# Optimization experiments

Measured on AMD Instinct MI355X. Metric: run time of the kernel, lower is better.

Reference implementation:

```python
import jax, jax.numpy as jnp
import numpy as np

B, T, C, H = 4, 2048, 1024, 16
HD = C // H  # head dim = 64


def setup_inputs() -> dict:
    key = jax.random.key(0)
    ks = jax.random.split(key, 5)
    s = 1.0 / np.sqrt(C)
    return {
        "x": jax.random.normal(ks[0], (B, T, C), jnp.float32),
        "Wk": jax.random.normal(ks[1], (C, C), jnp.float32) * s,
        "bk": jnp.zeros((C,), jnp.float32),
        "Wq": jax.random.normal(ks[2], (C, C), jnp.float32) * s,
        "bq": jnp.zeros((C,), jnp.float32),
        "Wv": jax.random.normal(ks[3], (C, C), jnp.float32) * s,
        "bv": jnp.zeros((C,), jnp.float32),
        "Wp": jax.random.normal(ks[4], (C, C), jnp.float32) * s,
        "bp": jnp.zeros((C,), jnp.float32),
    }


def reference(x, Wk, bk, Wq, bq, Wv, bv, Wp, bp):
    # Linear(in, out): y = x @ W.T + b  (W stored as [out, in], torch convention)
    k = (x @ Wk.T + bk).reshape(B, T, H, HD).transpose(0, 2, 1, 3)  # [B,H,T,HD]
    q = (x @ Wq.T + bq).reshape(B, T, H, HD).transpose(0, 2, 1, 3)
    v = (x @ Wv.T + bv).reshape(B, T, H, HD).transpose(0, 2, 1, 3)
    scale = 1.0 / np.sqrt(HD)
    att = jnp.einsum("bhqd,bhkd->bhqk", q, k) * scale  # [B,H,T,T]
    causal = jnp.tril(jnp.ones((T, T), bool))
    att = jnp.where(causal[None, None, :, :], att, -jnp.inf)
    att = jax.nn.softmax(att, axis=-1)
    y = jnp.einsum("bhqk,bhkd->bhqd", att, v)  # [B,H,T,HD]
    y = y.transpose(0, 2, 1, 3).reshape(B, T, C)
    return y @ Wp.T + bp
```

## Files before the change

### kernel.cpp

```cpp
#include <hip/hip_runtime.h>
#include <hip/hip_bf16.h>
#include <cmath>

#define Tt 2048
#define Cc 1024
#define Hh 16
#define HDd 64

typedef __attribute__((ext_vector_type(8))) short short8;
typedef __attribute__((ext_vector_type(4))) float f32x4;

#define ASYNC16(gp, lp)                                       \
    __builtin_amdgcn_global_load_lds(                         \
        (const __attribute__((address_space(1))) void*)(gp),  \
        (__attribute__((address_space(3))) void*)(lp), 16, 0, 0)

__device__ __forceinline__ unsigned short f32_bf16(float f) {
    unsigned u = __float_as_uint(f);
    u += 0x7FFF + ((u >> 16) & 1);
    return (unsigned short)(u >> 16);
}
__device__ __forceinline__ unsigned short f32_bf16_rn(float f) {
    return (unsigned short)((__float_as_uint(f) + 0x8000u) >> 16);
}
__device__ __forceinline__ float fast_exp2(float x) {
#if __has_builtin(__builtin_amdgcn_exp2f)
    return __builtin_amdgcn_exp2f(x);
#else
    return exp2f(x);
#endif
}

__global__ __launch_bounds__(256) void cvt_all(
    const float* __restrict__ x, const float* __restrict__ a,
    const float* __restrict__ b, const float* __restrict__ c,
    const float* __restrict__ d, unsigned short* __restrict__ ox,
    unsigned short* __restrict__ oa, unsigned short* __restrict__ ob,
    unsigned short* __restrict__ oc, unsigned short* __restrict__ od) {
    const int id = blockIdx.x * 256 + threadIdx.x;
    const float* src; unsigned short* dst; int sub;
    if (id < 2097152) {
        src = x; dst = ox; sub = id;
    } else {
        const int wi = id - 2097152;
        const int which = wi >> 18;
        sub = wi & 262143;
        if (which == 0)      { src = a; dst = oa; }
        else if (which == 1) { src = b; dst = ob; }
        else if (which == 2) { src = c; dst = oc; }
        else                 { src = d; dst = od; }
    }
    float4 v = ((const float4*)src)[sub];
    ushort4 o;
    o.x = f32_bf16(v.x); o.y = f32_bf16(v.y);
    o.z = f32_bf16(v.z); o.w = f32_bf16(v.w);
    ((ushort4*)dst)[sub] = o;
}

__global__ __launch_bounds__(256) void gemm_qkv(const unsigned short* __restrict__ A,
                                                const unsigned short* __restrict__ Wcat,
                                                const float* __restrict__ bq,
                                                const float* __restrict__ bk,
                                                const float* __restrict__ bv,
                                                unsigned short* __restrict__ qout,
                                                unsigned short* __restrict__ kout,
                                                unsigned short* __restrict__ vout) {
    __shared__ unsigned short sA[2][128 * 32];
    __shared__ unsigned short sB[2][128 * 32];

    const int tid  = threadIdx.x;
    const int bm0  = blockIdx.y * 128;
    const int bn0  = blockIdx.x * 128;
    const int wid  = tid >> 6;
    const int lane = tid & 63;
    const int quad = lane >> 4;
    const int lr   = lane & 15;
    const int wm   = (wid & 1) * 64;
    const int wn   = (wid >> 1) * 64;

    const int sr   = lane >> 2;
    const int scol = (lane & 3) * 8;
    const int row0 = wid * 16 + sr;
    const int row1 = 64 + wid * 16 + sr;
    const int lo0  = wid * 512;
    const int lo1  = (4 + wid) * 512;

    f32x4 acc[4][4];
    f32x4 zero = {0.f, 0.f, 0.f, 0.f};
#pragma unroll
    for (int i = 0; i < 4; i++)
#pragma unroll
        for (int j = 0; j < 4; j++) acc[i][j] = zero;

    ASYNC16(A    + (size_t)(bm0 + row0) * Cc + scol, sA[0] + lo0);
    ASYNC16(A    + (size_t)(bm0 + row1) * Cc + scol, sA[0] + lo1);
    ASYNC16(Wcat + (size_t)(bn0 + row0) * Cc + scol, sB[0] + lo0);
    ASYNC16(Wcat + (size_t)(bn0 + row1) * Cc + scol, sB[0] + lo1);
    __syncthreads();

    for (int kt = 0; kt < Cc / 32; ++kt) {
        const int cur = kt & 1, nxt = cur ^ 1;
        if (kt + 1 < Cc / 32) {
            const int kb = (kt + 1) * 32;
            ASYNC16(A    + (size_t)(bm0 + row0) * Cc + kb + scol, sA[nxt] + lo0);
            ASYNC16(A    + (size_t)(bm0 + row1) * Cc + kb + scol, sA[nxt] + lo1);
            ASYNC16(Wcat + (size_t)(bn0 + row0) * Cc + kb + scol, sB[nxt] + lo0);
            ASYNC16(Wcat + (size_t)(bn0 + row1) * Cc + kb + scol, sB[nxt] + lo1);
        }

        short8 af[4], bf[4];
#pragma unroll
        for (int i = 0; i < 4; i++)
            af[i] = *(const short8*)(sA[cur] + (wm + i * 16 + lr) * 32 + quad * 8);
#pragma unroll
        for (int j = 0; j < 4; j++)
            bf[j] = *(const short8*)(sB[cur] + (wn + j * 16 + lr) * 32 + quad * 8);
#pragma unroll
        for (int i = 0; i < 4; i++)
#pragma unroll
            for (int j = 0; j < 4; j++)
                acc[i][j] = __builtin_amdgcn_mfma_f32_16x16x32_bf16(af[i], bf[j], acc[i][j], 0, 0, 0);

        __syncthreads();
    }

    const int which = bn0 >> 10;
    const float* bias = (which == 0) ? bq : (which == 1) ? bk : bv;
    unsigned short* outp = (which == 0) ? qout : (which == 1) ? kout : vout;
    const float scale = (which == 0) ? 0.1803368801111204f : 1.0f;
    const bool vmode = (which == 2);
    const int nb = bn0 & 1023;

#pragma unroll
    for (int j = 0; j < 4; j++) {
        const int nl = nb + wn + j * 16 + lr;
        const float bvv = bias[nl];
        const int h = nl >> 6, hd = nl & 63;
#pragma unroll
        for (int i = 0; i < 4; i++) {
            const int m0 = bm0 + wm + i * 16 + quad * 4;
            const int b = m0 >> 11, t0 = m0 & 2047;
            if (vmode) {
                ushort4 pk;
                pk.x = f32_bf16_rn(acc[i][j][0] + bvv);
                pk.y = f32_bf16_rn(acc[i][j][1] + bvv);
                pk.z = f32_bf16_rn(acc[i][j][2] + bvv);
                pk.w = f32_bf16_rn(acc[i][j][3] + bvv);
                *(ushort4*)(outp + (((size_t)(b * Hh + h)) * HDd + hd) * Tt + t0) = pk;
            } else {
#pragma unroll
                for (int r = 0; r < 4; r++) {
                    const float val = (acc[i][j][r] + bvv) * scale;
                    outp[(((size_t)(b * Hh + h)) * Tt + t0 + r) * HDd + hd] =
                        f32_bf16_rn(val);
                }
            }
        }
    }
}

__global__ __launch_bounds__(256) void gemm_proj(const unsigned short* __restrict__ A,
                                                 const unsigned short* __restrict__ W,
                                                 const float* __restrict__ bias,
                                                 float* __restrict__ out) {
    __shared__ unsigned short sA[2][128 * 32];
    __shared__ unsigned short sB[2][64 * 32];

    const int tid  = threadIdx.x;
    const int bm0  = blockIdx.y * 128;
    const int bn0  = blockIdx.x * 64;
    const int wid  = tid >> 6;
    const int lane = tid & 63;
    const int quad = lane >> 4;
    const int lr   = lane & 15;
    const int wm   = (wid & 1) * 64;
    const int wn   = (wid >> 1) * 32;

    const int sr   = lane >> 2;
    const int scol = (lane & 3) * 8;
    const int row0 = wid * 16 + sr;
    const int row1 = 64 + wid * 16 + sr;
    const int lo0  = wid * 512;
    const int lo1  = (4 + wid) * 512;

    f32x4 acc[4][2];
    f32x4 zero = {0.f, 0.f, 0.f, 0.f};
#pragma unroll
    for (int i = 0; i < 4; i++)
#pragma unroll
        for (int j = 0; j < 2; j++) acc[i][j] = zero;

    ASYNC16(A + (size_t)(bm0 + row0) * Cc + scol, sA[0] + lo0);
    ASYNC16(A + (size_t)(bm0 + row1) * Cc + scol, sA[0] + lo1);
    ASYNC16(W + (size_t)(bn0 + row0) * Cc + scol, sB[0] + lo0);
    __syncthreads();

    for (int kt = 0; kt < Cc / 32; ++kt) {
        const int cur = kt & 1, nxt = cur ^ 1;
        if (kt + 1 < Cc / 32) {
            const int kb = (kt + 1) * 32;
            ASYNC16(A + (size_t)(bm0 + row0) * Cc + kb + scol, sA[nxt] + lo0);
            ASYNC16(A + (size_t)(bm0 + row1) * Cc + kb + scol, sA[nxt] + lo1);
            ASYNC16(W + (size_t)(bn0 + row0) * Cc + kb + scol, sB[nxt] + lo0);
        }

        short8 af[4], bf[2];
#pragma unroll
        for (int i = 0; i < 4; i++)
            af[i] = *(const short8*)(sA[cur] + (wm + i * 16 + lr) * 32 + quad * 8);
#pragma unroll
        for (int j = 0; j < 2; j++)
            bf[j] = *(const short8*)(sB[cur] + (wn + j * 16 + lr) * 32 + quad * 8);
#pragma unroll
        for (int i = 0; i < 4; i++)
#pragma unroll
            for (int j = 0; j < 2; j++)
                acc[i][j] = __builtin_amdgcn_mfma_f32_16x16x32_bf16(af[i], bf[j], acc[i][j], 0, 0, 0);

        __syncthreads();
    }

#pragma unroll
    for (int j = 0; j < 2; j++) {
        const int n = bn0 + wn + j * 16 + lr;
        const float bvv = bias[n];
#pragma unroll
        for (int i = 0; i < 4; i++)
#pragma unroll
            for (int r = 0; r < 4; r++) {
                const int m = bm0 + wm + i * 16 + quad * 4 + r;
                out[(size_t)m * Cc + n] = acc[i][j][r] + bvv;
            }
    }
}

__global__ __launch_bounds__(256) void attn(const unsigned short* __restrict__ q,
                                            const unsigned short* __restrict__ k,
                                            const unsigned short* __restrict__ vt,
                                            unsigned short* __restrict__ y) {
    __shared__ unsigned short sK[2][64 * 72];
    __shared__ unsigned short sV[2][64 * 72];
    __shared__ unsigned short sP[4][2][16 * 72];

    const int tid  = threadIdx.x;
    const int wid  = tid >> 6;
    const int lane = tid & 63;
    const int quad = lane >> 4;
    const int lr   = lane & 15;

    const int bh = blockIdx.y;
    const size_t headq = (size_t)bh * Tt * HDd;
    const unsigned short* kg = k + headq;
    const unsigned short* vg = vt + headq;
    const int b = bh >> 4, h = bh & 15;

    const int rs0 = tid >> 3;
    const int es  = (tid & 7) * 8;

    f32x4 zero = {0.f, 0.f, 0.f, 0.f};

    for (int pass = 0; pass < 2; ++pass) {
        const int qt = pass ? (15 - blockIdx.x) : blockIdx.x;
        const int qb = qt * 128;
        const int ntiles = 2 * qt + 2;

        short8 qf[2][2];
#pragma unroll
        for (int s = 0; s < 2; s++) {
            const unsigned short* qp =
                q + headq + (size_t)(qb + s * 64 + wid * 16 + lr) * HDd;
            qf[s][0] = *(const short8*)(qp + quad * 8);
            qf[s][1] = *(const short8*)(qp + 32 + quad * 8);
        }

        f32x4 o[2][4];
        float l_run[2][4];
#pragma unroll
        for (int s = 0; s < 2; s++)
#pragma unroll
            for (int i = 0; i < 4; i++) { o[s][i] = zero; l_run[s][i] = 0.f; }

        uint4 ka0 = *(const uint4*)(kg + (size_t)(rs0)      * HDd + es);
        uint4 ka1 = *(const uint4*)(kg + (size_t)(rs0 + 32) * HDd + es);
        uint4 va0 = *(const uint4*)(vg + (size_t)(rs0)      * Tt + es);
        uint4 va1 = *(const uint4*)(vg + (size_t)(rs0 + 32) * Tt + es);
        *(uint4*)(sK[0] + rs0 * 72 + es)        = ka0;
        *(uint4*)(sK[0] + (rs0 + 32) * 72 + es) = ka1;
        *(uint4*)(sV[0] + rs0 * 72 + es)        = va0;
        *(uint4*)(sV[0] + (rs0 + 32) * 72 + es) = va1;
        __syncthreads();
        {
            const int kb2 = 64;
            ka0 = *(const uint4*)(kg + (size_t)(kb2 + rs0)      * HDd + es);
            ka1 = *(const uint4*)(kg + (size_t)(kb2 + rs0 + 32) * HDd + es);
            va0 = *(const uint4*)(vg + (size_t)(rs0)      * Tt + kb2 + es);
            va1 = *(const uint4*)(vg + (size_t)(rs0 + 32) * Tt + kb2 + es);
        }

        for (int kt = 0; kt < ntiles; ++kt) {
            const int cur = kt & 1, nxt = cur ^ 1;
            if (kt + 1 < ntiles) {
                *(uint4*)(sK[nxt] + rs0 * 72 + es)        = ka0;
                *(uint4*)(sK[nxt] + (rs0 + 32) * 72 + es) = ka1;
                *(uint4*)(sV[nxt] + rs0 * 72 + es)        = va0;
                *(uint4*)(sV[nxt] + (rs0 + 32) * 72 + es) = va1;
            }
            if (kt + 2 < ntiles) {
                const int kb2 = (kt + 2) * 64;
                ka0 = *(const uint4*)(kg + (size_t)(kb2 + rs0)      * HDd + es);
                ka1 = *(const uint4*)(kg + (size_t)(kb2 + rs0 + 32) * HDd + es);
                va0 = *(const uint4*)(vg + (size_t)(rs0)      * Tt + kb2 + es);
                va1 = *(const uint4*)(vg + (size_t)(rs0 + 32) * Tt + kb2 + es);
            }

            const unsigned short* bK = sK[cur];
            const unsigned short* bV = sV[cur];
            const int s_lo = (kt == ntiles - 1) ? 1 : 0;

            f32x4 sc[2][4];
#pragma unroll
            for (int s = 0; s < 2; s++) {
                if (s < s_lo) continue;
#pragma unroll
                for (int nt = 0; nt < 4; nt++) {
                    short8 b0 = *(const short8*)(bK + (nt * 16 + lr) * 72 + quad * 8);
                    short8 b1 = *(const short8*)(bK + (nt * 16 + lr) * 72 + 32 + quad * 8);
                    f32x4 a = zero;
                    a = __builtin_amdgcn_mfma_f32_16x16x32_bf16(qf[s][0], b0, a, 0, 0, 0);
                    a = __builtin_amdgcn_mfma_f32_16x16x32_bf16(qf[s][1], b1, a, 0, 0, 0);
                    sc[s][nt] = a;
                }
            }

#pragma unroll
            for (int s = 0; s < 2; s++) {
                if (s < s_lo) continue;
                if (kt == ntiles - 2 + s) {
#pragma unroll
                    for (int nt = 0; nt < 4; nt++)
#pragma unroll
                        for (int r = 0; r < 4; r++)
                            sc[s][nt][r] = (nt * 16 + lr <= wid * 16 + quad * 4 + r)
                                               ? sc[s][nt][r] : -INFINITY;
                }
                unsigned short* sPw = sP[wid][s];
#pragma unroll
                for (int nt = 0; nt < 4; nt++)
#pragma unroll
                    for (int r = 0; r < 4; r++) {
                        const float p = fast_exp2(sc[s][nt][r]);
                        l_run[s][r] += p;
                        sPw[(quad * 4 + r) * 72 + nt * 16 + lr] = f32_bf16_rn(p);
                    }
            }

#pragma unroll
            for (int s = 0; s < 2; s++) {
                if (s < s_lo) continue;
                const unsigned short* sPw = sP[wid][s];
                short8 pa0 = *(const short8*)(sPw + lr * 72 + quad * 8);
                short8 pa1 = *(const short8*)(sPw + lr * 72 + 32 + quad * 8);
#pragma unroll
                for (int nt = 0; nt < 4; nt++) {
                    short8 vb0 = *(const short8*)(bV + (nt * 16 + lr) * 72 + quad * 8);
                    short8 vb1 = *(const short8*)(bV + (nt * 16 + lr) * 72 + 32 + quad * 8);
                    o[s][nt] = __builtin_amdgcn_mfma_f32_16x16x32_bf16(pa0, vb0, o[s][nt], 0, 0, 0);
                    o[s][nt] = __builtin_amdgcn_mfma_f32_16x16x32_bf16(pa1, vb1, o[s][nt], 0, 0, 0);
                }
            }

            __syncthreads();
        }

#pragma unroll
        for (int s = 0; s < 2; s++) {
#pragma unroll
            for (int r = 0; r < 4; r++) {
                float ls = l_run[s][r];
                ls += __shfl_xor(ls, 1);
                ls += __shfl_xor(ls, 2);
                ls += __shfl_xor(ls, 4);
                ls += __shfl_xor(ls, 8);
                const float inv = 1.0f / ls;
                const int t = qb + s * 64 + wid * 16 + quad * 4 + r;
#pragma unroll
                for (int nt = 0; nt < 4; nt++) {
                    const int dim = nt * 16 + lr;
                    y[((size_t)(b * Tt + t)) * Cc + h * HDd + dim] =
                        f32_bf16_rn(o[s][nt][r] * inv);
                }
            }
        }
    }
}

extern "C" void kernel_launch(void* const* d_in, const int* in_sizes, int n_in,
                              void* d_out, int out_size, void* d_ws, size_t ws_size,
                              hipStream_t stream) {
    const float* x  = (const float*)d_in[0];
    const float* Wk = (const float*)d_in[1];
    const float* bk = (const float*)d_in[2];
    const float* Wq = (const float*)d_in[3];
    const float* bq = (const float*)d_in[4];
    const float* Wv = (const float*)d_in[5];
    const float* bv = (const float*)d_in[6];
    const float* Wp = (const float*)d_in[7];
    const float* bp = (const float*)d_in[8];
    float* out = (float*)d_out;

    char* ws = (char*)d_ws;
    size_t off = 0;
    auto alloc = [&](size_t bytes) { char* p = ws + off; off += bytes; return p; };
    const size_t MK = (size_t)8192 * 1024;
    const size_t NK = (size_t)1024 * 1024;
    unsigned short* xb   = (unsigned short*)alloc(MK * 2);
    unsigned short* Wcat = (unsigned short*)alloc(3 * NK * 2);
    unsigned short* Wqb  = Wcat;
    unsigned short* Wkb  = Wcat + NK;
    unsigned short* Wvb  = Wcat + 2 * NK;
    unsigned short* Wpb  = (unsigned short*)alloc(NK * 2);
    unsigned short* qh   = (unsigned short*)alloc(MK * 2);
    unsigned short* kh   = (unsigned short*)alloc(MK * 2);
    unsigned short* vth  = (unsigned short*)alloc(MK * 2);
    unsigned short* ya   = (unsigned short*)alloc(MK * 2);

    cvt_all<<<12288, 256, 0, stream>>>(x, Wq, Wk, Wv, Wp, xb, Wqb, Wkb, Wvb, Wpb);

    gemm_qkv<<<dim3(24, 64), 256, 0, stream>>>(xb, Wcat, bq, bk, bv, qh, kh, vth);

    attn<<<dim3(8, 64), 256, 0, stream>>>(qh, kh, vth, ya);

    gemm_proj<<<dim3(16, 64), 256, 0, stream>>>(ya, Wpb, bp, out);
}
```

Measured before the change: 279.3 us.

## Rewrite QKV GEMM as 256x256 eight-wave pipelined kernel with swizzled LDS

Replaces the 128x128 four-wave QKV projection GEMM with a 256x256 tile, 512-thread kernel that uses K-steps of 64 and 128KB of dynamic LDS double-buffered in four quadrants. Global-to-LDS loads are interleaved with four MFMA phases under explicit barriers, s_setprio and waitcnt control. LDS columns are XOR-swizzled to avoid bank conflicts. The aim is more data reuse per byte loaded and better overlap of memory with MFMA work. The cost is higher register pressure and only 384 blocks, which could leave some CUs idle.

```diff
diff --git a/kernel.cpp b/kernel.cpp
--- a/kernel.cpp
+++ b/kernel.cpp
@@ -57,72 +57,142 @@
     ((ushort4*)dst)[sub] = o;
 }
 
-__global__ __launch_bounds__(256) void gemm_qkv(const unsigned short* __restrict__ A,
-                                                const unsigned short* __restrict__ Wcat,
-                                                const float* __restrict__ bq,
-                                                const float* __restrict__ bk,
-                                                const float* __restrict__ bv,
-                                                unsigned short* __restrict__ qout,
-                                                unsigned short* __restrict__ kout,
-                                                unsigned short* __restrict__ vout) {
-    __shared__ unsigned short sA[2][128 * 32];
-    __shared__ unsigned short sB[2][128 * 32];
+__global__ __launch_bounds__(512, 2) void gemm_qkv8(
+    const unsigned short* __restrict__ A,
+    const unsigned short* __restrict__ Wcat,
+    const float* __restrict__ bq, const float* __restrict__ bk,
+    const float* __restrict__ bv,
+    unsigned short* __restrict__ qout, unsigned short* __restrict__ kout,
+    unsigned short* __restrict__ vout) {
+    extern __shared__ unsigned short lds[];
 
     const int tid  = threadIdx.x;
-    const int bm0  = blockIdx.y * 128;
-    const int bn0  = blockIdx.x * 128;
     const int wid  = tid >> 6;
     const int lane = tid & 63;
     const int quad = lane >> 4;
     const int lr   = lane & 15;
-    const int wm   = (wid & 1) * 64;
-    const int wn   = (wid >> 1) * 64;
-
-    const int sr   = lane >> 2;
-    const int scol = (lane & 3) * 8;
-    const int row0 = wid * 16 + sr;
-    const int row1 = 64 + wid * 16 + sr;
-    const int lo0  = wid * 512;
-    const int lo1  = (4 + wid) * 512;
-
-    f32x4 acc[4][4];
-    f32x4 zero = {0.f, 0.f, 0.f, 0.f};
-#pragma unroll
-    for (int i = 0; i < 4; i++)
-#pragma unroll
-        for (int j = 0; j < 4; j++) acc[i][j] = zero;
-
-    ASYNC16(A    + (size_t)(bm0 + row0) * Cc + scol, sA[0] + lo0);
-    ASYNC16(A    + (size_t)(bm0 + row1) * Cc + scol, sA[0] + lo1);
-    ASYNC16(Wcat + (size_t)(bn0 + row0) * Cc + scol, sB[0] + lo0);
-    ASYNC16(Wcat + (size_t)(bn0 + row1) * Cc + scol, sB[0] + lo1);
-    __syncthreads();
-
-    for (int kt = 0; kt < Cc / 32; ++kt) {
-        const int cur = kt & 1, nxt = cur ^ 1;
-        if (kt + 1 < Cc / 32) {
-            const int kb = (kt + 1) * 32;
-            ASYNC16(A    + (size_t)(bm0 + row0) * Cc + kb + scol, sA[nxt] + lo0);
-            ASYNC16(A    + (size_t)(bm0 + row1) * Cc + kb + scol, sA[nxt] + lo1);
-            ASYNC16(Wcat + (size_t)(bn0 + row0) * Cc + kb + scol, sB[nxt] + lo0);
-            ASYNC16(Wcat + (size_t)(bn0 + row1) * Cc + kb + scol, sB[nxt] + lo1);
-        }
-
-        short8 af[4], bf[4];
-#pragma unroll
-        for (int i = 0; i < 4; i++)
-            af[i] = *(const short8*)(sA[cur] + (wm + i * 16 + lr) * 32 + quad * 8);
-#pragma unroll
-        for (int j = 0; j < 4; j++)
-            bf[j] = *(const short8*)(sB[cur] + (wn + j * 16 + lr) * 32 + quad * 8);
-#pragma unroll
-        for (int i = 0; i < 4; i++)
-#pragma unroll
-            for (int j = 0; j < 4; j++)
-                acc[i][j] = __builtin_amdgcn_mfma_f32_16x16x32_bf16(af[i], bf[j], acc[i][j], 0, 0, 0);
-
-        __syncthreads();
-    }
+    const int wr   = wid >> 2;
+    const int wc   = wid & 3;
+
+    const int bm0 = blockIdx.y * 256;
+    const int bn0 = blockIdx.x * 256;
+
+    const int srow  = wid * 8 + (lane >> 3);
+    const int scol  = ((lane & 7) ^ (lane >> 3)) * 8;
+    const int sldso = wid * 512;
+
+    const int a_r   = wr * 64 + lr;
+    const int b_r   = wc * 32 + lr;
+    const int slot0 = (quad ^ (lr & 7)) * 8;
+    const int slot1 = ((quad ^ 4) ^ (lr & 7)) * 8;
+
+    f32x4 acc[8][4];
+    const f32x4 zero = {0.f, 0.f, 0.f, 0.f};
+#pragma unroll
+    for (int i = 0; i < 8; ++i)
+#pragma unroll
+        for (int j = 0; j < 4; ++j) acc[i][j] = zero;
+
+    short8 areg[4][2];
+    short8 breg[2][2][2];
+
+#define STG(S, BUF, REG, GB, GROW)                                          \
+    do {                                                                    \
+        if ((S) < 16) {                                                     \
+            unsigned short* lb = lds + ((BUF) * 4 + (REG)) * 8192 + sldso;  \
+            const unsigned short* gp =                                      \
+                (GB) + (size_t)((GROW) + srow) * Cc + (S) * 64 + scol;      \
+            ASYNC16(gp, lb);                                                \
+            ASYNC16(gp + (size_t)64 * Cc, lb + 4096);                       \
+        }                                                                   \
+    } while (0)
+
+#define LDA(mh)                                                             \
+    do {                                                                    \
+        const unsigned short* ab = bufb + (mh) * 8192;                      \
+        _Pragma("unroll") for (int mf = 0; mf < 4; ++mf) {                  \
+            areg[mf][0] = *(const short8*)(ab + (a_r + mf * 16) * 64 + slot0); \
+            areg[mf][1] = *(const short8*)(ab + (a_r + mf * 16) * 64 + slot1); \
+        }                                                                   \
+    } while (0)
+
+#define LDB(nh)                                                             \
+    do {                                                                    \
+        const unsigned short* bb = bufb + (2 + (nh)) * 8192;                \
+        _Pragma("unroll") for (int nf = 0; nf < 2; ++nf) {                  \
+            breg[nh][nf][0] = *(const short8*)(bb + (b_r + nf * 16) * 64 + slot0); \
+            breg[nh][nf][1] = *(const short8*)(bb + (b_r + nf * 16) * 64 + slot1); \
+        }                                                                   \
+    } while (0)
+
+#define MFMA_PHASE(mh, nh)                                                  \
+    _Pragma("unroll") for (int mf = 0; mf < 4; ++mf)                        \
+    _Pragma("unroll") for (int nf = 0; nf < 2; ++nf) {                      \
+        acc[(mh)*4+mf][(nh)*2+nf] = __builtin_amdgcn_mfma_f32_16x16x32_bf16( \
+            areg[mf][0], breg[nh][nf][0], acc[(mh)*4+mf][(nh)*2+nf], 0,0,0); \
+        acc[(mh)*4+mf][(nh)*2+nf] = __builtin_amdgcn_mfma_f32_16x16x32_bf16( \
+            areg[mf][1], breg[nh][nf][1], acc[(mh)*4+mf][(nh)*2+nf], 0,0,0); \
+    }
+
+#define TILE(T, BC, WN)                                                     \
+    {                                                                       \
+        const unsigned short* bufb = lds + (BC) * 32768;                    \
+        LDA(0);                                                             \
+        LDB(0);                                                             \
+        STG((T) + 1, (BC) ^ 1, 1, A, bm0 + 128);                            \
+        __builtin_amdgcn_s_barrier();                                       \
+        asm volatile("s_waitcnt lgkmcnt(0)" ::: "memory");                  \
+        __builtin_amdgcn_s_setprio(1);                                      \
+        MFMA_PHASE(0, 0);                                                   \
+        __builtin_amdgcn_s_setprio(0);                                      \
+        __builtin_amdgcn_s_barrier();                                       \
+        LDB(1);                                                             \
+        STG((T) + 1, (BC) ^ 1, 3, Wcat, bn0 + 128);                         \
+        __builtin_amdgcn_s_barrier();                                       \
+        asm volatile("s_waitcnt lgkmcnt(0)" ::: "memory");                  \
+        __builtin_amdgcn_s_setprio(1);                                      \
+        MFMA_PHASE(0, 1);                                                   \
+        __builtin_amdgcn_s_setprio(0);                                      \
+        __builtin_amdgcn_s_barrier();                                       \
+        LDA(1);                                                             \
+        STG((T) + 2, (BC), 0, A, bm0);                                      \
+        __builtin_amdgcn_s_barrier();                                       \
+        asm volatile("s_waitcnt lgkmcnt(0)" ::: "memory");                  \
+        __builtin_amdgcn_s_setprio(1);                                      \
+        MFMA_PHASE(1, 0);                                                   \
+        __builtin_amdgcn_s_setprio(0);                                      \
+        __builtin_amdgcn_s_barrier();                                       \
+        STG((T) + 2, (BC), 2, Wcat, bn0);                                   \
+        __builtin_amdgcn_s_barrier();                                       \
+        __builtin_amdgcn_s_setprio(1);                                      \
+        MFMA_PHASE(1, 1);                                                   \
+        __builtin_amdgcn_s_setprio(0);                                      \
+        asm volatile("s_waitcnt vmcnt(" #WN ")" ::: "memory");              \
+        __builtin_amdgcn_s_barrier();                                       \
+    }
+
+    STG(0, 0, 0, A, bm0);
+    STG(0, 0, 1, A, bm0 + 128);
+    STG(0, 0, 2, Wcat, bn0);
+    STG(0, 0, 3, Wcat, bn0 + 128);
+    STG(1, 1, 0, A, bm0);
+    STG(1, 1, 2, Wcat, bn0);
+    asm volatile("s_waitcnt vmcnt(4)" ::: "memory");
+    __builtin_amdgcn_s_barrier();
+
+    for (int t2 = 0; t2 < 7; ++t2) {
+        const int T0 = t2 * 2;
+        TILE(T0, 0, 4);
+        TILE(T0 + 1, 1, 4);
+    }
+    TILE(14, 0, 0);
+    TILE(15, 1, 0);
+
+#undef TILE
+#undef MFMA_PHASE
+#undef LDB
+#undef LDA
+#undef STG
 
     const int which = bn0 >> 10;
     const float* bias = (which == 0) ? bq : (which == 1) ? bk : bv;
@@ -132,31 +202,35 @@
     const int nb = bn0 & 1023;
 
 #pragma unroll
-    for (int j = 0; j < 4; j++) {
-        const int nl = nb + wn + j * 16 + lr;
-        const float bvv = bias[nl];
-        const int h = nl >> 6, hd = nl & 63;
-#pragma unroll
-        for (int i = 0; i < 4; i++) {
-            const int m0 = bm0 + wm + i * 16 + quad * 4;
-            const int b = m0 >> 11, t0 = m0 & 2047;
-            if (vmode) {
-                ushort4 pk;
-                pk.x = f32_bf16_rn(acc[i][j][0] + bvv);
-                pk.y = f32_bf16_rn(acc[i][j][1] + bvv);
-                pk.z = f32_bf16_rn(acc[i][j][2] + bvv);
-                pk.w = f32_bf16_rn(acc[i][j][3] + bvv);
-                *(ushort4*)(outp + (((size_t)(b * Hh + h)) * HDd + hd) * Tt + t0) = pk;
-            } else {
-#pragma unroll
-                for (int r = 0; r < 4; r++) {
-                    const float val = (acc[i][j][r] + bvv) * scale;
-                    outp[(((size_t)(b * Hh + h)) * Tt + t0 + r) * HDd + hd] =
-                        f32_bf16_rn(val);
+    for (int nh = 0; nh < 2; ++nh)
+#pragma unroll
+        for (int nf = 0; nf < 2; ++nf) {
+            const int nl = nb + nh * 128 + wc * 32 + nf * 16 + lr;
+            const float bvv = bias[nl];
+            const int h = nl >> 6, hd = nl & 63;
+#pragma unroll
+            for (int mh = 0; mh < 2; ++mh)
+#pragma unroll
+                for (int mf = 0; mf < 4; ++mf) {
+                    const f32x4 a = acc[mh * 4 + mf][nh * 2 + nf];
+                    const int m0 = bm0 + mh * 128 + wr * 64 + mf * 16 + quad * 4;
+                    const int b = m0 >> 11, t0 = m0 & 2047;
+                    if (vmode) {
+                        ushort4 pk;
+                        pk.x = f32_bf16_rn(a[0] + bvv);
+                        pk.y = f32_bf16_rn(a[1] + bvv);
+                        pk.z = f32_bf16_rn(a[2] + bvv);
+                        pk.w = f32_bf16_rn(a[3] + bvv);
+                        *(ushort4*)(outp + (((size_t)(b * Hh + h)) * HDd + hd) * Tt + t0) = pk;
+                    } else {
+#pragma unroll
+                        for (int r = 0; r < 4; ++r) {
+                            outp[(((size_t)(b * Hh + h)) * Tt + t0 + r) * HDd + hd] =
+                                f32_bf16_rn((a[r] + bvv) * scale);
+                        }
+                    }
                 }
-            }
         }
-    }
 }
 
 __global__ __launch_bounds__(256) void gemm_proj(const unsigned short* __restrict__ A,
@@ -424,9 +498,17 @@
     unsigned short* vth  = (unsigned short*)alloc(MK * 2);
     unsigned short* ya   = (unsigned short*)alloc(MK * 2);
 
+    static bool lds_attr_set = false;
+    if (!lds_attr_set) {
+        (void)hipFuncSetAttribute((const void*)gemm_qkv8,
+                                  hipFuncAttributeMaxDynamicSharedMemorySize,
+                                  131072);
+        lds_attr_set = true;
+    }
+
     cvt_all<<<12288, 256, 0, stream>>>(x, Wq, Wk, Wv, Wp, xb, Wqb, Wkb, Wvb, Wpb);
 
-    gemm_qkv<<<dim3(24, 64), 256, 0, stream>>>(xb, Wcat, bq, bk, bv, qh, kh, vth);
+    gemm_qkv8<<<dim3(12, 32), 512, 131072, stream>>>(xb, Wcat, bq, bk, bv, qh, kh, vth);
 
     attn<<<dim3(8, 64), 256, 0, stream>>>(qh, kh, vth, ya);
 
```

After: 268.4 us. 3.9% less time.
